# Kernel optimization log

Hardware: AMD Instinct MI355X
Metric: run time of the kernel (lower is better)

## Reference

```python
import jax, jax.numpy as jnp
import numpy as np

B, N, E = 128, 256, 2048
BINS = 16

def _gcn(x, src, dst, W, b):
    # GCNConv with self-loops and symmetric deg^-1/2 normalization (PyG default).
    h = x @ W  # [N, Fout]
    deg = jnp.zeros(x.shape[0], x.dtype).at[dst].add(1.0) + 1.0  # +1 self-loop
    dinv = jax.lax.rsqrt(deg)
    coef = dinv[src] * dinv[dst]  # [E]
    agg = jnp.zeros_like(h).at[dst].add(h[src] * coef[:, None])
    return agg + h / deg[:, None] + b  # self-loop norm = 1/deg

def _gnn(x, ei, W1, b1, W2, b2, W3, b3):
    # x: [B,N,Fin], ei: [B,2,E]. Dropout skipped (eval mode).
    def single(x, ei):
        s, d = ei[0], ei[1]
        h = jax.nn.relu(_gcn(x, s, d, W1, b1))
        h = jax.nn.relu(_gcn(h, s, d, W2, b2))
        return _gcn(h, s, d, W3, b3)
    return jax.vmap(single)(x, ei)

def _att_pool(x, Watt):
    # SimGNN attention pooling; all graphs have exactly N nodes.
    ctx = jnp.tanh((x @ Watt.T).sum(axis=1) / jnp.asarray(N, x.dtype))  # [B,f3]
    scores = jax.nn.sigmoid(jnp.einsum('bnf,bf->bn', x, ctx))  # [B,N]
    return jnp.einsum('bnf,bn->bf', x, scores)  # [B,f3]

def _forward(xq, xc, eq, ec, W1, b1, W2, b2, W3, b3, Watt, ntnW, ntnV, ntnb, fc1W, fc1b, fc2W, fc2b):
    q = _gnn(xq, eq, W1, b1, W2, b2, W3, b3)  # [B,N,f3]
    c = _gnn(xc, ec, W1, b1, W2, b2, W3, b3)
    e1 = _att_pool(q, Watt)
    e2 = _att_pool(c, Watt)
    # NTN: bilinear + linear on concat + bias
    scores = jax.nn.relu(
        jnp.einsum('bi,tij,bj->bt', e1, ntnW, e2)
        + jnp.concatenate([e1, e2], axis=-1) @ ntnV.T
        + ntnb
    )  # [B, tensor_neurons]
    # histogram of all pairwise node-embedding dot products (torch.histc semantics)
    s = jnp.einsum('bnf,bmf->bnm', q, c).ravel()
    lo, hi = s.min(), s.max()
    idx = jnp.clip(jnp.floor((s - lo) / (hi - lo) * BINS).astype(jnp.int32), 0, BINS - 1)
    counts = jnp.zeros(BINS, s.dtype).at[idx].add(1.0)
    h = jax.lax.stop_gradient(counts / counts.sum())
    scores = jnp.concatenate([scores, jnp.broadcast_to(h, (scores.shape[0], BINS))], axis=1)
    scores = jax.nn.relu(scores @ fc1W.T + fc1b)
    p = jax.nn.sigmoid(scores @ fc2W.T + fc2b)  # [B,1]
    return p.squeeze()


def setup_inputs() -> dict:
    key = jax.random.key(0)
    ks = jax.random.split(key, 20)
    Fin, f1, f2, f3, T, BN = 128, 128, 64, 32, 16, 16
    def xav(k, shape):
        fan_in, fan_out = shape[-1], shape[0]
        lim = np.sqrt(6.0 / (fan_in + fan_out))
        return jax.random.uniform(k, shape, jnp.float32, -lim, lim)
    return {
        'xq': jax.random.normal(ks[0], (B, N, Fin), jnp.float32),
        'xc': jax.random.normal(ks[1], (B, N, Fin), jnp.float32),
        'eq': jax.random.randint(ks[2], (B, 2, E), 0, N, jnp.int32),
        'ec': jax.random.randint(ks[3], (B, 2, E), 0, N, jnp.int32),
        'W1': xav(ks[4], (Fin, f1)), 'b1': jnp.zeros((f1,), jnp.float32),
        'W2': xav(ks[5], (f1, f2)), 'b2': jnp.zeros((f2,), jnp.float32),
        'W3': xav(ks[6], (f2, f3)), 'b3': jnp.zeros((f3,), jnp.float32),
        'Watt': xav(ks[7], (f3, f3)),
        'ntnW': xav(ks[8], (T, f3, f3)),
        'ntnV': xav(ks[9], (T, 2 * f3)),
        'ntnb': xav(ks[10], (T, 1)).squeeze(-1),
        'fc1W': xav(ks[11], (BN, T + BINS)), 'fc1b': jnp.zeros((BN,), jnp.float32),
        'fc2W': xav(ks[12], (1, BN)), 'fc2b': jnp.zeros((1,), jnp.float32),
    }


def reference(xq, xc, eq, ec, W1, b1, W2, b2, W3, b3, Watt, ntnW, ntnV, ntnb, fc1W, fc1b, fc2W, fc2b):
    return _forward(xq, xc, eq, ec, W1, b1, W2, b2, W3, b3, Watt, ntnW, ntnV, ntnb, fc1W, fc1b, fc2W, fc2b)
```

## Files before the change

### kernel.cpp

```cpp
#include <hip/hip_runtime.h>
#include <math.h>

#define BB 128
#define NN 256
#define EE 2048
#define BINS 16

typedef unsigned short u16;

__global__ void csr_kernel(const int* __restrict__ eq, const int* __restrict__ ec,
                           int* __restrict__ off, u16* __restrict__ srcs,
                           float* __restrict__ dvsg) {
    int g = blockIdx.x;
    int b = g < BB ? g : g - BB;
    const int* ei = g < BB ? eq : ec;
    int t = threadIdx.x;
    __shared__ int cnt[NN];
    __shared__ int sa[NN], sb[NN];
    __shared__ int cursor[NN];
    cnt[t] = 0;
    __syncthreads();
    const int* src = ei + b * 2 * EE;
    const int* dst = src + EE;
    for (int e = t; e < EE; e += 256) atomicAdd(&cnt[dst[e]], 1);
    __syncthreads();
    dvsg[g * NN + t] = rsqrtf((float)cnt[t] + 1.0f);
    sa[t] = cnt[t];
    __syncthreads();
    int* pin = sa; int* pout = sb;
    for (int d = 1; d < NN; d <<= 1) {
        int v = pin[t];
        if (t >= d) v += pin[t - d];
        pout[t] = v;
        __syncthreads();
        int* tmp = pin; pin = pout; pout = tmp;
    }
    int excl = pin[t] - cnt[t];
    off[g * 257 + t] = excl;
    if (t == 255) off[g * 257 + 256] = EE;
    cursor[t] = excl;
    __syncthreads();
    for (int e = t; e < EE; e += 256) {
        int d = dst[e], s = src[e];
        int pos = atomicAdd(&cursor[d], 1);
        srcs[g * EE + pos] = (u16)s;
    }
}

template<int FIN, int FOUT, bool RELU, int NSPLIT>
__global__ __launch_bounds__(512) void gcn_fused4(
        const float* __restrict__ X0, const float* __restrict__ X1,
        const float* __restrict__ W, const float* __restrict__ bias,
        const int* __restrict__ off, const u16* __restrict__ srcs,
        const float* __restrict__ dvsg, float* __restrict__ OUT) {
    constexpr int CHUNKS = FOUT / 32;
    int blk = blockIdx.x;
    int g = blk % (2 * BB);
    int rest = blk / (2 * BB);
    int cb = (rest % CHUNKS) * 32;
    int half = rest / CHUNKS;
    int t = threadIdx.x;

    __shared__ float uni[NN * 33];
    __shared__ int   eoff[NN + 1];
    __shared__ u16   esrc[EE];
    __shared__ float dvs_s[NN];
    float* xsT = uni;
    float* wt  = uni + 16 * 260;
    float* hT  = uni;

    const float* xg = (g < BB) ? (X0 + (size_t)g * NN * FIN)
                               : (X1 + (size_t)(g - BB) * NN * FIN);
    const int* o = off + g * 257;
    const u16* sr = srcs + (size_t)g * EE;

    for (int i = t; i < EE; i += 512) esrc[i] = sr[i];
    for (int i = t; i <= NN; i += 512) eoff[i] = o[i];
    if (t < NN) dvs_s[t] = dvsg[g * NN + t];

    int l = t & 63;
    int wv = t >> 6;

    float acc[4][4];
#pragma unroll
    for (int i = 0; i < 4; i++)
#pragma unroll
        for (int j = 0; j < 4; j++) acc[i][j] = 0.f;

    int sn = t >> 1, qk = (t & 1) * 8;
    const float* xr = xg + sn * FIN + qk;
    float4 v0 = *(const float4*)xr;
    float4 v1 = *(const float4*)(xr + 4);
    float wreg = W[(t >> 5) * FOUT + cb + (t & 31)];

    for (int k0 = 0; k0 < FIN; k0 += 16) {
        xsT[(qk + 0) * 260 + sn] = v0.x;
        xsT[(qk + 1) * 260 + sn] = v0.y;
        xsT[(qk + 2) * 260 + sn] = v0.z;
        xsT[(qk + 3) * 260 + sn] = v0.w;
        xsT[(qk + 4) * 260 + sn] = v1.x;
        xsT[(qk + 5) * 260 + sn] = v1.y;
        xsT[(qk + 6) * 260 + sn] = v1.z;
        xsT[(qk + 7) * 260 + sn] = v1.w;
        wt[t] = wreg;
        __syncthreads();
        if (k0 + 16 < FIN) {
            xr += 16;
            v0 = *(const float4*)xr;
            v1 = *(const float4*)(xr + 4);
            wreg = W[(k0 + 16 + (t >> 5)) * FOUT + cb + (t & 31)];
        }
#pragma unroll
        for (int k = 0; k < 16; k++) {
            float4 xv = *(const float4*)&xsT[k * 260 + 4 * l];
            float4 wvv = *(const float4*)&wt[k * 32 + 4 * wv];
            acc[0][0] += xv.x * wvv.x; acc[0][1] += xv.x * wvv.y;
            acc[0][2] += xv.x * wvv.z; acc[0][3] += xv.x * wvv.w;
            acc[1][0] += xv.y * wvv.x; acc[1][1] += xv.y * wvv.y;
            acc[1][2] += xv.y * wvv.z; acc[1][3] += xv.y * wvv.w;
            acc[2][0] += xv.z * wvv.x; acc[2][1] += xv.z * wvv.y;
            acc[2][2] += xv.z * wvv.z; acc[2][3] += xv.z * wvv.w;
            acc[3][0] += xv.w * wvv.x; acc[3][1] += xv.w * wvv.y;
            acc[3][2] += xv.w * wvv.z; acc[3][3] += xv.w * wvv.w;
        }
        __syncthreads();
    }
#pragma unroll
    for (int i = 0; i < 4; i++)
#pragma unroll
        for (int j = 0; j < 4; j++)
            hT[(4 * l + i) * 33 + 4 * wv + j] = acc[i][j];
    __syncthreads();

    int c = t & 31, ng = t >> 5;
    float bb_ = bias[cb + c];
    float* outp = OUT + (size_t)g * NN * FOUT;
    constexpr int NSEG = NN / NSPLIT;
    int nlo = half * NSEG, nhi = nlo + NSEG;
    for (int n = nlo + ng; n < nhi; n += 16) {
        int j0 = eoff[n], j1 = eoff[n + 1];
        float dn = dvs_s[n];
        float a = 0.f;
        int j = j0;
        for (; j + 1 < j1; j += 2) {
            int s0 = esrc[j], s1 = esrc[j + 1];
            a += hT[s0 * 33 + c] * (dvs_s[s0] * dn);
            a += hT[s1 * 33 + c] * (dvs_s[s1] * dn);
        }
        if (j < j1) {
            int s0 = esrc[j];
            a += hT[s0 * 33 + c] * (dvs_s[s0] * dn);
        }
        float d0i = 1.0f / ((float)(j1 - j0) + 1.0f);
        float val = a + hT[n * 33 + c] * d0i + bb_;
        if (RELU) val = fmaxf(val, 0.f);
        outp[n * FOUT + cb + c] = val;
    }
}

__global__ void attpool_kernel(const float* __restrict__ X, const float* __restrict__ Watt,
                               float* __restrict__ e) {
    int g = blockIdx.x;
    int t = threadIdx.x;
    __shared__ float xs[NN * 33];
    __shared__ float red[256];
    __shared__ float mean_s[32], ctx_s[32], sc[NN];
    const float* x = X + (size_t)g * NN * 32;
    for (int i = t; i < NN * 32; i += 256) { int n = i >> 5, c = i & 31; xs[n * 33 + c] = x[i]; }
    __syncthreads();
    {
        int c = t & 31, p = t >> 5;
        float s = 0.f;
        for (int n = p * 32; n < (p + 1) * 32; n++) s += xs[n * 33 + c];
        red[t] = s;
    }
    __syncthreads();
    if (t < 32) {
        float m = 0.f;
        for (int p = 0; p < 8; p++) m += red[p * 32 + t];
        mean_s[t] = m / (float)NN;
    }
    __syncthreads();
    if (t < 32) {
        float a = 0.f;
        for (int f = 0; f < 32; f++) a += mean_s[f] * Watt[t * 32 + f];
        ctx_s[t] = tanhf(a);
    }
    __syncthreads();
    {
        float a = 0.f;
        for (int f = 0; f < 32; f++) a += xs[t * 33 + f] * ctx_s[f];
        sc[t] = 1.f / (1.f + expf(-a));
    }
    __syncthreads();
    {
        int c = t & 31, p = t >> 5;
        float s = 0.f;
        for (int n = p * 32; n < (p + 1) * 32; n++) s += xs[n * 33 + c] * sc[n];
        red[t] = s;
    }
    __syncthreads();
    if (t < 32) {
        float s = 0.f;
        for (int p = 0; p < 8; p++) s += red[p * 32 + t];
        e[g * 32 + t] = s;
    }
}

#define PD_STAGE_AND_DOT \
    int blk = blockIdx.x; \
    int b = blk >> 2; \
    int tq = (blk >> 1) & 1, tc = blk & 1; \
    __shared__ float qsT[32 * 132]; \
    __shared__ float csT[32 * 132]; \
    int t = threadIdx.x; \
    { \
        int n = t >> 1, f0 = (t & 1) * 16; \
        const float* qp = Q + ((size_t)b * NN + tq * 128 + n) * 32 + f0; \
        const float* cp = C + ((size_t)b * NN + tc * 128 + n) * 32 + f0; \
        float qa16[16], ca16[16]; \
        *(float4*)&qa16[0]  = *(const float4*)(qp); \
        *(float4*)&qa16[4]  = *(const float4*)(qp + 4); \
        *(float4*)&qa16[8]  = *(const float4*)(qp + 8); \
        *(float4*)&qa16[12] = *(const float4*)(qp + 12); \
        *(float4*)&ca16[0]  = *(const float4*)(cp); \
        *(float4*)&ca16[4]  = *(const float4*)(cp + 4); \
        *(float4*)&ca16[8]  = *(const float4*)(cp + 8); \
        *(float4*)&ca16[12] = *(const float4*)(cp + 12); \
        _Pragma("unroll") \
        for (int m = 0; m < 16; m++) { \
            qsT[(f0 + m) * 132 + n] = qa16[m]; \
            csT[(f0 + m) * 132 + n] = ca16[m]; \
        } \
    } \
    __syncthreads(); \
    int rg = (t >> 4) * 4, cg = (t & 15) * 4; \
    float acc[8][8]; \
    _Pragma("unroll") \
    for (int i = 0; i < 8; i++) \
        _Pragma("unroll") \
        for (int j = 0; j < 8; j++) acc[i][j] = 0.f; \
    _Pragma("unroll 2") \
    for (int f = 0; f < 32; f++) { \
        float4 qa = *(const float4*)&qsT[f * 132 + rg]; \
        float4 qb = *(const float4*)&qsT[f * 132 + 64 + rg]; \
        float4 ca = *(const float4*)&csT[f * 132 + cg]; \
        float4 cb = *(const float4*)&csT[f * 132 + 64 + cg]; \
        float qv[8] = {qa.x, qa.y, qa.z, qa.w, qb.x, qb.y, qb.z, qb.w}; \
        float cv[8] = {ca.x, ca.y, ca.z, ca.w, cb.x, cb.y, cb.z, cb.w}; \
        _Pragma("unroll") \
        for (int i = 0; i < 8; i++) \
            _Pragma("unroll") \
            for (int j = 0; j < 8; j++) acc[i][j] += qv[i] * cv[j]; \
    }

__global__ __launch_bounds__(256, 4) void pairdot_minmax(
        const float* __restrict__ Q, const float* __restrict__ C,
        float* __restrict__ bmin, float* __restrict__ bmax) {
    PD_STAGE_AND_DOT
    float lmin = acc[0][0], lmax = acc[0][0];
#pragma unroll
    for (int i = 0; i < 8; i++)
#pragma unroll
        for (int j = 0; j < 8; j++) {
            lmin = fminf(lmin, acc[i][j]);
            lmax = fmaxf(lmax, acc[i][j]);
        }
    __shared__ float rmin[256], rmax[256];
    rmin[t] = lmin; rmax[t] = lmax;
    __syncthreads();
    for (int s = 128; s > 0; s >>= 1) {
        if (t < s) { rmin[t] = fminf(rmin[t], rmin[t + s]); rmax[t] = fmaxf(rmax[t], rmax[t + s]); }
        __syncthreads();
    }
    if (t == 0) { bmin[blk] = rmin[0]; bmax[blk] = rmax[0]; }
}

__global__ void minmax_kernel(const float* __restrict__ bmin, const float* __restrict__ bmax,
                              float* __restrict__ lohi, float* __restrict__ counts) {
    __shared__ float rmin[256], rmax[256];
    int t = threadIdx.x;
    float lmin = 1e30f, lmax = -1e30f;
    for (int i = t; i < 512; i += 256) { lmin = fminf(lmin, bmin[i]); lmax = fmaxf(lmax, bmax[i]); }
    rmin[t] = lmin; rmax[t] = lmax;
    __syncthreads();
    for (int s = 128; s > 0; s >>= 1) {
        if (t < s) { rmin[t] = fminf(rmin[t], rmin[t + s]); rmax[t] = fmaxf(rmax[t], rmax[t + s]); }
        __syncthreads();
    }
    if (t == 0) { lohi[0] = rmin[0]; lohi[1] = rmax[0]; }
    if (t < BINS) counts[t] = 0.f;
}

__global__ __launch_bounds__(256, 4) void pairdot_hist(
        const float* __restrict__ Q, const float* __restrict__ C,
        const float* __restrict__ lohi, float* __restrict__ counts) {
    PD_STAGE_AND_DOT
    float lo = lohi[0], hi = lohi[1];
    float scale = (float)BINS / (hi - lo);
    int lane = t & 63;
    int cnt = 0;
#pragma unroll
    for (int i = 0; i < 8; i++)
#pragma unroll
        for (int j = 0; j < 8; j++) {
            int idx = (int)floorf((acc[i][j] - lo) * scale);
            idx = min(max(idx, 0), BINS - 1);
            unsigned long long b0 = __ballot((idx & 1) != 0);
            unsigned long long b1 = __ballot((idx & 2) != 0);
            unsigned long long b2 = __ballot((idx & 4) != 0);
            unsigned long long b3 = __ballot((idx & 8) != 0);
            unsigned long long msk = ((lane & 1) ? b0 : ~b0);
            msk &= ((lane & 2) ? b1 : ~b1);
            msk &= ((lane & 4) ? b2 : ~b2);
            msk &= ((lane & 8) ? b3 : ~b3);
            cnt += __popcll(msk);
        }
    __shared__ float wbins[4][BINS];
    int wave = t >> 6;
    if (lane < BINS) wbins[wave][lane] = (float)cnt;
    __syncthreads();
    if (t < BINS) {
        atomicAdd(&counts[t], wbins[0][t] + wbins[1][t] + wbins[2][t] + wbins[3][t]);
    }
}

__global__ void final_kernel(const float* __restrict__ e1, const float* __restrict__ e2,
                             const float* __restrict__ ntnW, const float* __restrict__ ntnV,
                             const float* __restrict__ ntnb, const float* __restrict__ counts,
                             const float* __restrict__ fc1W, const float* __restrict__ fc1b,
                             const float* __restrict__ fc2W, const float* __restrict__ fc2b,
                             float* __restrict__ out) {
    int b = blockIdx.x;
    int t = threadIdx.x;
    __shared__ float a1[32], a2[32], red[256], z[32], u[16];
    if (t < 32) a1[t] = e1[b * 32 + t];
    else if (t < 64) a2[t - 32] = e2[b * 32 + t - 32];
    __syncthreads();
    int tt = t >> 4, g = t & 15;
    float p = 0.f;
#pragma unroll
    for (int ii = 0; ii < 2; ii++) {
        int i = g + 16 * ii;
        float d = 0.f;
        const float* wr = ntnW + (tt * 32 + i) * 32;
        for (int j = 0; j < 32; j++) d += wr[j] * a2[j];
        p += a1[i] * d;
    }
    red[t] = p;
    __syncthreads();
    if (t < 16) {
        float s = 0.f;
        for (int g2 = 0; g2 < 16; g2++) s += red[t * 16 + g2];
        float lin = ntnb[t];
        for (int i = 0; i < 32; i++) lin += ntnV[t * 64 + i] * a1[i];
        for (int i = 0; i < 32; i++) lin += ntnV[t * 64 + 32 + i] * a2[i];
        z[t] = fmaxf(s + lin, 0.f);
    } else if (t < 32) {
        float tot = 0.f;
        for (int i = 0; i < BINS; i++) tot += counts[i];
        z[t] = counts[t - 16] / tot;
    }
    __syncthreads();
    if (t < 16) {
        float a = fc1b[t];
        for (int i = 0; i < 32; i++) a += fc1W[t * 32 + i] * z[i];
        u[t] = fmaxf(a, 0.f);
    }
    __syncthreads();
    if (t == 0) {
        float a = fc2b[0];
        for (int i = 0; i < 16; i++) a += fc2W[i] * u[i];
        out[b] = 1.f / (1.f + expf(-a));
    }
}

extern "C" void kernel_launch(void* const* d_in, const int* in_sizes, int n_in,
                              void* d_out, int out_size, void* d_ws, size_t ws_size,
                              hipStream_t stream) {
    const float* xq   = (const float*)d_in[0];
    const float* xc   = (const float*)d_in[1];
    const int*   eq   = (const int*)d_in[2];
    const int*   ec   = (const int*)d_in[3];
    const float* W1   = (const float*)d_in[4];
    const float* b1   = (const float*)d_in[5];
    const float* W2   = (const float*)d_in[6];
    const float* b2   = (const float*)d_in[7];
    const float* W3   = (const float*)d_in[8];
    const float* b3   = (const float*)d_in[9];
    const float* Watt = (const float*)d_in[10];
    const float* ntnW = (const float*)d_in[11];
    const float* ntnV = (const float*)d_in[12];
    const float* ntnb = (const float*)d_in[13];
    const float* fc1W = (const float*)d_in[14];
    const float* fc1b = (const float*)d_in[15];
    const float* fc2W = (const float*)d_in[16];
    const float* fc2b = (const float*)d_in[17];
    float* out = (float*)d_out;
    float* ws  = (float*)d_ws;

    float* O3   = ws;
    float* e12  = O3 + 2097152;
    float* bmin = e12 + 8192;
    float* bmax = bmin + 2048;
    float* lohi = bmax + 2048;
    float* cntw = lohi + 2;
    int*   off  = (int*)(ws + 2109504);
    u16*   srcs = (u16*)(off + 65792);
    float* dvsg = ws + 2437440;
    float* O1   = ws + 3223872;
    float* O2   = O1 + 8388608;

    float* O3Q = O3;
    float* O3C = O3 + (size_t)BB * NN * 32;
    float* e1w = e12;
    float* e2w = e12 + BB * 32;

    csr_kernel<<<2 * BB, 256, 0, stream>>>(eq, ec, off, srcs, dvsg);

    gcn_fused4<128, 128, true, 1><<<4 * 2 * BB, 512, 0, stream>>>(
        xq, xc, W1, b1, off, srcs, dvsg, O1);
    gcn_fused4<128, 64, true, 1><<<2 * 2 * BB, 512, 0, stream>>>(
        O1, O1 + (size_t)BB * NN * 128, W2, b2, off, srcs, dvsg, O2);
    gcn_fused4<64, 32, false, 2><<<2 * 2 * BB, 512, 0, stream>>>(
        O2, O2 + (size_t)BB * NN * 64, W3, b3, off, srcs, dvsg, O3);

    attpool_kernel<<<2 * BB, 256, 0, stream>>>(O3, Watt, e12);

    pairdot_minmax<<<BB * 4, 256, 0, stream>>>(O3Q, O3C, bmin, bmax);
    minmax_kernel<<<1, 256, 0, stream>>>(bmin, bmax, lohi, cntw);
    pairdot_hist<<<BB * 4, 256, 0, stream>>>(O3Q, O3C, lohi, cntw);

    final_kernel<<<BB, 256, 0, stream>>>(e1w, e2w, ntnW, ntnV, ntnb, cntw,
                                         fc1W, fc1b, fc2W, fc2b, out);
}
```

Measured before the change: 299.5 us.

## Widen GCN output chunk per block to cut redundant X GEMM reloads

Generalizes the fused GCN kernel to a configurable output-column chunk (64 instead of 32), so each block computes more output columns per load of X and layers 1 and 2 re-read the input fewer times. Layer 2 and 3 change how the aggregation work is split across blocks (more node splits), which recomputes the full GEMM in more blocks for layer 3 and layer 2. Larger chunks double register accumulators and shared memory, which may reduce occupancy.

Result: slower. 334.6 us (+11.7%).

```diff
diff --git a/kernel.cpp b/kernel.cpp
--- a/kernel.cpp
+++ b/kernel.cpp
@@ -47,21 +47,24 @@
     }
 }
 
-template<int FIN, int FOUT, bool RELU, int NSPLIT>
-__global__ __launch_bounds__(512) void gcn_fused4(
+template<int FIN, int FOUT, int CHUNK, bool RELU, int NSPLIT>
+__global__ __launch_bounds__(512) void gcn_fused5(
         const float* __restrict__ X0, const float* __restrict__ X1,
         const float* __restrict__ W, const float* __restrict__ bias,
         const int* __restrict__ off, const u16* __restrict__ srcs,
         const float* __restrict__ dvsg, float* __restrict__ OUT) {
-    constexpr int CHUNKS = FOUT / 32;
+    constexpr int CHUNKS = FOUT / CHUNK;
+    constexpr int CPW = CHUNK / 8;
+    constexpr int NPANEL = CHUNK / 32;
+    constexpr int PSTR = NN * 33;
     int blk = blockIdx.x;
     int g = blk % (2 * BB);
     int rest = blk / (2 * BB);
-    int cb = (rest % CHUNKS) * 32;
+    int cb = (rest % CHUNKS) * CHUNK;
     int half = rest / CHUNKS;
     int t = threadIdx.x;
 
-    __shared__ float uni[NN * 33];
+    __shared__ float uni[PSTR * NPANEL];
     __shared__ int   eoff[NN + 1];
     __shared__ u16   esrc[EE];
     __shared__ float dvs_s[NN];
@@ -81,17 +84,27 @@
     int l = t & 63;
     int wv = t >> 6;
 
-    float acc[4][4];
+    float acc[4][CPW];
 #pragma unroll
     for (int i = 0; i < 4; i++)
 #pragma unroll
-        for (int j = 0; j < 4; j++) acc[i][j] = 0.f;
+        for (int j = 0; j < CPW; j++) acc[i][j] = 0.f;
 
     int sn = t >> 1, qk = (t & 1) * 8;
     const float* xr = xg + sn * FIN + qk;
     float4 v0 = *(const float4*)xr;
     float4 v1 = *(const float4*)(xr + 4);
-    float wreg = W[(t >> 5) * FOUT + cb + (t & 31)];
+
+    constexpr int EPT = CHUNK / 32;
+    int wrow = t >> 5;
+    int wcol = (t & 31) * EPT;
+    float wreg[EPT];
+    if (EPT == 2) {
+        float2 w2 = *(const float2*)&W[(size_t)wrow * FOUT + cb + wcol];
+        wreg[0] = w2.x; wreg[1] = w2.y;
+    } else {
+        wreg[0] = W[(size_t)wrow * FOUT + cb + wcol];
+    }
 
     for (int k0 = 0; k0 < FIN; k0 += 16) {
         xsT[(qk + 0) * 260 + sn] = v0.x;
@@ -102,57 +115,72 @@
         xsT[(qk + 5) * 260 + sn] = v1.y;
         xsT[(qk + 6) * 260 + sn] = v1.z;
         xsT[(qk + 7) * 260 + sn] = v1.w;
-        wt[t] = wreg;
+        if (EPT == 2) *(float2*)&wt[wrow * CHUNK + wcol] = make_float2(wreg[0], wreg[1]);
+        else          wt[wrow * CHUNK + wcol] = wreg[0];
         __syncthreads();
         if (k0 + 16 < FIN) {
             xr += 16;
             v0 = *(const float4*)xr;
             v1 = *(const float4*)(xr + 4);
-            wreg = W[(k0 + 16 + (t >> 5)) * FOUT + cb + (t & 31)];
+            if (EPT == 2) {
+                float2 w2 = *(const float2*)&W[(size_t)(k0 + 16 + wrow) * FOUT + cb + wcol];
+                wreg[0] = w2.x; wreg[1] = w2.y;
+            } else {
+                wreg[0] = W[(size_t)(k0 + 16 + wrow) * FOUT + cb + wcol];
+            }
         }
 #pragma unroll
         for (int k = 0; k < 16; k++) {
             float4 xv = *(const float4*)&xsT[k * 260 + 4 * l];
-            float4 wvv = *(const float4*)&wt[k * 32 + 4 * wv];
-            acc[0][0] += xv.x * wvv.x; acc[0][1] += xv.x * wvv.y;
-            acc[0][2] += xv.x * wvv.z; acc[0][3] += xv.x * wvv.w;
-            acc[1][0] += xv.y * wvv.x; acc[1][1] += xv.y * wvv.y;
-            acc[1][2] += xv.y * wvv.z; acc[1][3] += xv.y * wvv.w;
-            acc[2][0] += xv.z * wvv.x; acc[2][1] += xv.z * wvv.y;
-            acc[2][2] += xv.z * wvv.z; acc[2][3] += xv.z * wvv.w;
-            acc[3][0] += xv.w * wvv.x; acc[3][1] += xv.w * wvv.y;
-            acc[3][2] += xv.w * wvv.z; acc[3][3] += xv.w * wvv.w;
+            float wc[CPW];
+#pragma unroll
+            for (int j4 = 0; j4 < CPW; j4 += 4) {
+                float4 w4 = *(const float4*)&wt[k * CHUNK + CPW * wv + j4];
+                wc[j4] = w4.x; wc[j4 + 1] = w4.y; wc[j4 + 2] = w4.z; wc[j4 + 3] = w4.w;
+            }
+            float xq4[4] = {xv.x, xv.y, xv.z, xv.w};
+#pragma unroll
+            for (int i = 0; i < 4; i++)
+#pragma unroll
+                for (int j = 0; j < CPW; j++) acc[i][j] += xq4[i] * wc[j];
         }
         __syncthreads();
     }
-#pragma unroll
-    for (int i = 0; i < 4; i++)
-#pragma unroll
-        for (int j = 0; j < 4; j++)
-            hT[(4 * l + i) * 33 + 4 * wv + j] = acc[i][j];
-    __syncthreads();
-
-    int c = t & 31, ng = t >> 5;
+    {
+        int colg = CPW * wv;
+        int p = colg >> 5, cw = colg & 31;
+#pragma unroll
+        for (int i = 0; i < 4; i++)
+#pragma unroll
+            for (int j4 = 0; j4 < CPW; j4 += 4)
+                *(float4*)&hT[p * PSTR + (4 * l + i) * 33 + cw + j4] =
+                    make_float4(acc[i][j4], acc[i][j4 + 1], acc[i][j4 + 2], acc[i][j4 + 3]);
+    }
+    __syncthreads();
+
+    constexpr int NG = 512 / CHUNK;
+    int c = t & (CHUNK - 1), ng = t / CHUNK;
+    int cp = c >> 5, cc = c & 31;
     float bb_ = bias[cb + c];
     float* outp = OUT + (size_t)g * NN * FOUT;
     constexpr int NSEG = NN / NSPLIT;
     int nlo = half * NSEG, nhi = nlo + NSEG;
-    for (int n = nlo + ng; n < nhi; n += 16) {
+    for (int n = nlo + ng; n < nhi; n += NG) {
         int j0 = eoff[n], j1 = eoff[n + 1];
         float dn = dvs_s[n];
         float a = 0.f;
         int j = j0;
         for (; j + 1 < j1; j += 2) {
             int s0 = esrc[j], s1 = esrc[j + 1];
-            a += hT[s0 * 33 + c] * (dvs_s[s0] * dn);
-            a += hT[s1 * 33 + c] * (dvs_s[s1] * dn);
+            a += hT[cp * PSTR + s0 * 33 + cc] * (dvs_s[s0] * dn);
+            a += hT[cp * PSTR + s1 * 33 + cc] * (dvs_s[s1] * dn);
         }
         if (j < j1) {
             int s0 = esrc[j];
-            a += hT[s0 * 33 + c] * (dvs_s[s0] * dn);
+            a += hT[cp * PSTR + s0 * 33 + cc] * (dvs_s[s0] * dn);
         }
         float d0i = 1.0f / ((float)(j1 - j0) + 1.0f);
-        float val = a + hT[n * 33 + c] * d0i + bb_;
+        float val = a + hT[cp * PSTR + n * 33 + cc] * d0i + bb_;
         if (RELU) val = fmaxf(val, 0.f);
         outp[n * FOUT + cb + c] = val;
     }
@@ -418,11 +446,11 @@
 
     csr_kernel<<<2 * BB, 256, 0, stream>>>(eq, ec, off, srcs, dvsg);
 
-    gcn_fused4<128, 128, true, 1><<<4 * 2 * BB, 512, 0, stream>>>(
+    gcn_fused5<128, 128, 64, true, 1><<<2 * 2 * BB, 512, 0, stream>>>(
         xq, xc, W1, b1, off, srcs, dvsg, O1);
-    gcn_fused4<128, 64, true, 1><<<2 * 2 * BB, 512, 0, stream>>>(
+    gcn_fused5<128, 64, 64, true, 2><<<2 * 2 * BB, 512, 0, stream>>>(
         O1, O1 + (size_t)BB * NN * 128, W2, b2, off, srcs, dvsg, O2);
-    gcn_fused4<64, 32, false, 2><<<2 * 2 * BB, 512, 0, stream>>>(
+    gcn_fused5<64, 32, 32, false, 4><<<4 * 2 * BB, 512, 0, stream>>>(
         O2, O2 + (size_t)BB * NN * 64, W3, b3, off, srcs, dvsg, O3);
 
     attpool_kernel<<<2 * BB, 256, 0, stream>>>(O3, Watt, e12);
```

## Double-buffer GCN GEMM staging and precompute per-edge normalization weights

Applied to the files above, without the earlier changes.

The GCN transform loop now keeps two shared-memory stages and prefetches global tiles two steps ahead in registers. This lets staging of the next tile overlap compute on the current one and removes a barrier per step. Separately, the CSR build kernel precomputes each edge's dinv[src]*dinv[dst] weight into a per-graph array, so the aggregation does one shared read instead of two lookups plus a multiply. The cost is more shared memory, more live registers and a larger edge-weight buffer in the workspace.

Measured after the change: 299.6 us. No clear change (+0.0%).

```diff
diff --git a/kernel.cpp b/kernel.cpp
--- a/kernel.cpp
+++ b/kernel.cpp
@@ -10,7 +10,7 @@
 
 __global__ void csr_kernel(const int* __restrict__ eq, const int* __restrict__ ec,
                            int* __restrict__ off, u16* __restrict__ srcs,
-                           float* __restrict__ dvsg) {
+                           float* __restrict__ wts) {
     int g = blockIdx.x;
     int b = g < BB ? g : g - BB;
     const int* ei = g < BB ? eq : ec;
@@ -18,13 +18,14 @@
     __shared__ int cnt[NN];
     __shared__ int sa[NN], sb[NN];
     __shared__ int cursor[NN];
+    __shared__ float dvs[NN];
     cnt[t] = 0;
     __syncthreads();
     const int* src = ei + b * 2 * EE;
     const int* dst = src + EE;
     for (int e = t; e < EE; e += 256) atomicAdd(&cnt[dst[e]], 1);
     __syncthreads();
-    dvsg[g * NN + t] = rsqrtf((float)cnt[t] + 1.0f);
+    dvs[t] = rsqrtf((float)cnt[t] + 1.0f);
     sa[t] = cnt[t];
     __syncthreads();
     int* pin = sa; int* pout = sb;
@@ -44,16 +45,19 @@
         int d = dst[e], s = src[e];
         int pos = atomicAdd(&cursor[d], 1);
         srcs[g * EE + pos] = (u16)s;
+        wts[g * EE + pos] = dvs[s] * dvs[d];
     }
 }
 
 template<int FIN, int FOUT, bool RELU, int NSPLIT>
-__global__ __launch_bounds__(512) void gcn_fused4(
+__global__ __launch_bounds__(512) void gcn_fused6(
         const float* __restrict__ X0, const float* __restrict__ X1,
         const float* __restrict__ W, const float* __restrict__ bias,
         const int* __restrict__ off, const u16* __restrict__ srcs,
-        const float* __restrict__ dvsg, float* __restrict__ OUT) {
+        const float* __restrict__ wts, float* __restrict__ OUT) {
     constexpr int CHUNKS = FOUT / 32;
+    constexpr int NW = FIN / 16;
+    constexpr int BUF = 16 * 260 + 16 * 32;
     int blk = blockIdx.x;
     int g = blk % (2 * BB);
     int rest = blk / (2 * BB);
@@ -61,22 +65,20 @@
     int half = rest / CHUNKS;
     int t = threadIdx.x;
 
-    __shared__ float uni[NN * 33];
+    __shared__ float uni[2 * BUF];
     __shared__ int   eoff[NN + 1];
     __shared__ u16   esrc[EE];
-    __shared__ float dvs_s[NN];
-    float* xsT = uni;
-    float* wt  = uni + 16 * 260;
-    float* hT  = uni;
+    __shared__ float ewt[EE];
+    float* hT = uni;
 
     const float* xg = (g < BB) ? (X0 + (size_t)g * NN * FIN)
                                : (X1 + (size_t)(g - BB) * NN * FIN);
     const int* o = off + g * 257;
     const u16* sr = srcs + (size_t)g * EE;
-
-    for (int i = t; i < EE; i += 512) esrc[i] = sr[i];
+    const float* wg = wts + (size_t)g * EE;
+
+    for (int i = t; i < EE; i += 512) { esrc[i] = sr[i]; ewt[i] = wg[i]; }
     for (int i = t; i <= NN; i += 512) eoff[i] = o[i];
-    if (t < NN) dvs_s[t] = dvsg[g * NN + t];
 
     int l = t & 63;
     int wv = t >> 6;
@@ -89,31 +91,58 @@
 
     int sn = t >> 1, qk = (t & 1) * 8;
     const float* xr = xg + sn * FIN + qk;
-    float4 v0 = *(const float4*)xr;
-    float4 v1 = *(const float4*)(xr + 4);
-    float wreg = W[(t >> 5) * FOUT + cb + (t & 31)];
-
-    for (int k0 = 0; k0 < FIN; k0 += 16) {
-        xsT[(qk + 0) * 260 + sn] = v0.x;
-        xsT[(qk + 1) * 260 + sn] = v0.y;
-        xsT[(qk + 2) * 260 + sn] = v0.z;
-        xsT[(qk + 3) * 260 + sn] = v0.w;
-        xsT[(qk + 4) * 260 + sn] = v1.x;
-        xsT[(qk + 5) * 260 + sn] = v1.y;
-        xsT[(qk + 6) * 260 + sn] = v1.z;
-        xsT[(qk + 7) * 260 + sn] = v1.w;
-        wt[t] = wreg;
-        __syncthreads();
-        if (k0 + 16 < FIN) {
-            xr += 16;
-            v0 = *(const float4*)xr;
-            v1 = *(const float4*)(xr + 4);
-            wreg = W[(k0 + 16 + (t >> 5)) * FOUT + cb + (t & 31)];
+    int wrow = t >> 5, wcol = t & 31;
+
+    auto stage = [&](float* buf, const float4& s0, const float4& s1, float sw) {
+        buf[(qk + 0) * 260 + sn] = s0.x;
+        buf[(qk + 1) * 260 + sn] = s0.y;
+        buf[(qk + 2) * 260 + sn] = s0.z;
+        buf[(qk + 3) * 260 + sn] = s0.w;
+        buf[(qk + 4) * 260 + sn] = s1.x;
+        buf[(qk + 5) * 260 + sn] = s1.y;
+        buf[(qk + 6) * 260 + sn] = s1.z;
+        buf[(qk + 7) * 260 + sn] = s1.w;
+        buf[16 * 260 + t] = sw;
+    };
+
+    float4 rA0 = *(const float4*)(xr);
+    float4 rA1 = *(const float4*)(xr + 4);
+    float  wA  = W[(size_t)wrow * FOUT + cb + wcol];
+    float4 rB0 = *(const float4*)(xr + 16);
+    float4 rB1 = *(const float4*)(xr + 20);
+    float  wB  = W[(size_t)(16 + wrow) * FOUT + cb + wcol];
+    stage(uni, rA0, rA1, wA);
+    if (NW > 2) {
+        rA0 = *(const float4*)(xr + 32);
+        rA1 = *(const float4*)(xr + 36);
+        wA  = W[(size_t)(32 + wrow) * FOUT + cb + wcol];
+    }
+    __syncthreads();
+
+#pragma unroll
+    for (int it = 0; it < NW; ++it) {
+        float* cur = uni + (it & 1) * BUF;
+        if (it + 1 < NW) {
+            float* nb = uni + ((it + 1) & 1) * BUF;
+            if (((it + 1) & 1) == 0) stage(nb, rA0, rA1, wA);
+            else                     stage(nb, rB0, rB1, wB);
+            if (it + 3 < NW) {
+                int ko = (it + 3) * 16;
+                if (((it + 3) & 1) == 0) {
+                    rA0 = *(const float4*)(xr + ko);
+                    rA1 = *(const float4*)(xr + ko + 4);
+                    wA  = W[(size_t)(ko + wrow) * FOUT + cb + wcol];
+                } else {
+                    rB0 = *(const float4*)(xr + ko);
+                    rB1 = *(const float4*)(xr + ko + 4);
+                    wB  = W[(size_t)(ko + wrow) * FOUT + cb + wcol];
+                }
+            }
         }
 #pragma unroll
         for (int k = 0; k < 16; k++) {
-            float4 xv = *(const float4*)&xsT[k * 260 + 4 * l];
-            float4 wvv = *(const float4*)&wt[k * 32 + 4 * wv];
+            float4 xv  = *(const float4*)&cur[k * 260 + 4 * l];
+            float4 wvv = *(const float4*)&cur[16 * 260 + k * 32 + 4 * wv];
             acc[0][0] += xv.x * wvv.x; acc[0][1] += xv.x * wvv.y;
             acc[0][2] += xv.x * wvv.z; acc[0][3] += xv.x * wvv.w;
             acc[1][0] += xv.y * wvv.x; acc[1][1] += xv.y * wvv.y;
@@ -139,17 +168,15 @@
     int nlo = half * NSEG, nhi = nlo + NSEG;
     for (int n = nlo + ng; n < nhi; n += 16) {
         int j0 = eoff[n], j1 = eoff[n + 1];
-        float dn = dvs_s[n];
         float a = 0.f;
         int j = j0;
         for (; j + 1 < j1; j += 2) {
             int s0 = esrc[j], s1 = esrc[j + 1];
-            a += hT[s0 * 33 + c] * (dvs_s[s0] * dn);
-            a += hT[s1 * 33 + c] * (dvs_s[s1] * dn);
+            a += hT[s0 * 33 + c] * ewt[j];
+            a += hT[s1 * 33 + c] * ewt[j + 1];
         }
         if (j < j1) {
-            int s0 = esrc[j];
-            a += hT[s0 * 33 + c] * (dvs_s[s0] * dn);
+            a += hT[esrc[j] * 33 + c] * ewt[j];
         }
         float d0i = 1.0f / ((float)(j1 - j0) + 1.0f);
         float val = a + hT[n * 33 + c] * d0i + bb_;
@@ -407,7 +434,7 @@
     float* cntw = lohi + 2;
     int*   off  = (int*)(ws + 2109504);
     u16*   srcs = (u16*)(off + 65792);
-    float* dvsg = ws + 2437440;
+    float* wts  = ws + 2437440;
     float* O1   = ws + 3223872;
     float* O2   = O1 + 8388608;
 
@@ -416,14 +443,14 @@
     float* e1w = e12;
     float* e2w = e12 + BB * 32;
 
-    csr_kernel<<<2 * BB, 256, 0, stream>>>(eq, ec, off, srcs, dvsg);
-
-    gcn_fused4<128, 128, true, 1><<<4 * 2 * BB, 512, 0, stream>>>(
-        xq, xc, W1, b1, off, srcs, dvsg, O1);
-    gcn_fused4<128, 64, true, 1><<<2 * 2 * BB, 512, 0, stream>>>(
-        O1, O1 + (size_t)BB * NN * 128, W2, b2, off, srcs, dvsg, O2);
-    gcn_fused4<64, 32, false, 2><<<2 * 2 * BB, 512, 0, stream>>>(
-        O2, O2 + (size_t)BB * NN * 64, W3, b3, off, srcs, dvsg, O3);
+    csr_kernel<<<2 * BB, 256, 0, stream>>>(eq, ec, off, srcs, wts);
+
+    gcn_fused6<128, 128, true, 1><<<4 * 2 * BB, 512, 0, stream>>>(
+        xq, xc, W1, b1, off, srcs, wts, O1);
+    gcn_fused6<128, 64, true, 1><<<2 * 2 * BB, 512, 0, stream>>>(
+        O1, O1 + (size_t)BB * NN * 128, W2, b2, off, srcs, wts, O2);
+    gcn_fused6<64, 32, false, 2><<<2 * 2 * BB, 512, 0, stream>>>(
+        O2, O2 + (size_t)BB * NN * 64, W3, b3, off, srcs, wts, O3);
 
     attpool_kernel<<<2 * BB, 256, 0, stream>>>(O3, Watt, e12);
 
```

## Fuse all three GCN layers into one per-graph kernel with precomputed edge weights

Applied to the files above, without the earlier changes.

The three separate GCN layer launches are replaced by a single 1024-thread block per graph. That block computes X@W1, aggregation, X@W2, aggregation, X@W3 and the final aggregation, keeping the intermediate activations in registers and shared memory instead of writing O1 and O2 to global memory. The CSR kernel now precomputes per-edge normalisation weights dinv[s]*dinv[d], which removes the per-edge multiply and the lookup during aggregation. The cost is lower grid parallelism: 256 blocks instead of up to 2048, with heavy shared memory and register use per block, which may limit occupancy.

After: 757.0 us. 2.53x slower.

```diff
diff --git a/kernel.cpp b/kernel.cpp
--- a/kernel.cpp
+++ b/kernel.cpp
@@ -10,7 +10,7 @@
 
 __global__ void csr_kernel(const int* __restrict__ eq, const int* __restrict__ ec,
                            int* __restrict__ off, u16* __restrict__ srcs,
-                           float* __restrict__ dvsg) {
+                           float* __restrict__ wts) {
     int g = blockIdx.x;
     int b = g < BB ? g : g - BB;
     const int* ei = g < BB ? eq : ec;
@@ -18,13 +18,14 @@
     __shared__ int cnt[NN];
     __shared__ int sa[NN], sb[NN];
     __shared__ int cursor[NN];
+    __shared__ float dvs[NN];
     cnt[t] = 0;
     __syncthreads();
     const int* src = ei + b * 2 * EE;
     const int* dst = src + EE;
     for (int e = t; e < EE; e += 256) atomicAdd(&cnt[dst[e]], 1);
     __syncthreads();
-    dvsg[g * NN + t] = rsqrtf((float)cnt[t] + 1.0f);
+    dvs[t] = rsqrtf((float)cnt[t] + 1.0f);
     sa[t] = cnt[t];
     __syncthreads();
     int* pin = sa; int* pout = sb;
@@ -44,117 +45,219 @@
         int d = dst[e], s = src[e];
         int pos = atomicAdd(&cursor[d], 1);
         srcs[g * EE + pos] = (u16)s;
-    }
-}
-
-template<int FIN, int FOUT, bool RELU, int NSPLIT>
-__global__ __launch_bounds__(512) void gcn_fused4(
-        const float* __restrict__ X0, const float* __restrict__ X1,
-        const float* __restrict__ W, const float* __restrict__ bias,
+        wts[g * EE + pos] = dvs[s] * dvs[d];
+    }
+}
+
+__global__ __launch_bounds__(1024) void gcn_all(
+        const float* __restrict__ XQ, const float* __restrict__ XC,
+        const float* __restrict__ W1, const float* __restrict__ b1,
+        const float* __restrict__ W2, const float* __restrict__ b2,
+        const float* __restrict__ W3, const float* __restrict__ b3,
         const int* __restrict__ off, const u16* __restrict__ srcs,
-        const float* __restrict__ dvsg, float* __restrict__ OUT) {
-    constexpr int CHUNKS = FOUT / 32;
-    int blk = blockIdx.x;
-    int g = blk % (2 * BB);
-    int rest = blk / (2 * BB);
-    int cb = (rest % CHUNKS) * 32;
-    int half = rest / CHUNKS;
+        const float* __restrict__ wts, float* __restrict__ O3) {
+    int g = blockIdx.x;
     int t = threadIdx.x;
 
-    __shared__ float uni[NN * 33];
+    __shared__ float Hb[NN * 67];
+    __shared__ float xsT[16 * 260];
+    __shared__ float wts_s[16 * 64];
     __shared__ int   eoff[NN + 1];
     __shared__ u16   esrc[EE];
-    __shared__ float dvs_s[NN];
-    float* xsT = uni;
-    float* wt  = uni + 16 * 260;
-    float* hT  = uni;
-
-    const float* xg = (g < BB) ? (X0 + (size_t)g * NN * FIN)
-                               : (X1 + (size_t)(g - BB) * NN * FIN);
-    const int* o = off + g * 257;
-    const u16* sr = srcs + (size_t)g * EE;
-
-    for (int i = t; i < EE; i += 512) esrc[i] = sr[i];
-    for (int i = t; i <= NN; i += 512) eoff[i] = o[i];
-    if (t < NN) dvs_s[t] = dvsg[g * NN + t];
+    __shared__ float ewt[EE];
+
+    const float* xg = (g < BB) ? (XQ + (size_t)g * NN * 128)
+                               : (XC + (size_t)(g - BB) * NN * 128);
+    {
+        const int* o = off + g * 257;
+        const u16* sre = srcs + (size_t)g * EE;
+        const float* wge = wts + (size_t)g * EE;
+        for (int i = t; i < EE; i += 1024) { esrc[i] = sre[i]; ewt[i] = wge[i]; }
+        if (t <= NN) eoff[t] = o[t];
+    }
 
     int l = t & 63;
     int wv = t >> 6;
-
-    float acc[4][4];
-#pragma unroll
-    for (int i = 0; i < 4; i++)
-#pragma unroll
-        for (int j = 0; j < 4; j++) acc[i][j] = 0.f;
-
-    int sn = t >> 1, qk = (t & 1) * 8;
-    const float* xr = xg + sn * FIN + qk;
-    float4 v0 = *(const float4*)xr;
-    float4 v1 = *(const float4*)(xr + 4);
-    float wreg = W[(t >> 5) * FOUT + cb + (t & 31)];
-
-    for (int k0 = 0; k0 < FIN; k0 += 16) {
-        xsT[(qk + 0) * 260 + sn] = v0.x;
-        xsT[(qk + 1) * 260 + sn] = v0.y;
-        xsT[(qk + 2) * 260 + sn] = v0.z;
-        xsT[(qk + 3) * 260 + sn] = v0.w;
-        xsT[(qk + 4) * 260 + sn] = v1.x;
-        xsT[(qk + 5) * 260 + sn] = v1.y;
-        xsT[(qk + 6) * 260 + sn] = v1.z;
-        xsT[(qk + 7) * 260 + sn] = v1.w;
-        wt[t] = wreg;
+    int sr_ = t >> 2;
+    int sq  = (t & 3) * 4;
+    int wr16 = t >> 6, wc64 = t & 63;
+    int gc = t & 63, gng = t >> 6;
+    const float* xrow = xg + sr_ * 128 + sq;
+
+    float a1[2][16];
+    float a2[16];
+
+#pragma unroll
+    for (int hf = 0; hf < 2; ++hf) {
+        const int cb = hf * 64;
+        float acc[4][4];
+#pragma unroll
+        for (int i = 0; i < 4; i++)
+#pragma unroll
+            for (int j = 0; j < 4; j++) acc[i][j] = 0.f;
+        float4 xv4 = *(const float4*)(xrow);
+        float wreg = W1[(size_t)wr16 * 128 + cb + wc64];
+        for (int k0 = 0; k0 < 128; k0 += 16) {
+            xsT[(sq + 0) * 260 + sr_] = xv4.x;
+            xsT[(sq + 1) * 260 + sr_] = xv4.y;
+            xsT[(sq + 2) * 260 + sr_] = xv4.z;
+            xsT[(sq + 3) * 260 + sr_] = xv4.w;
+            wts_s[t] = wreg;
+            __syncthreads();
+            if (k0 + 16 < 128) {
+                xv4 = *(const float4*)(xrow + k0 + 16);
+                wreg = W1[(size_t)(k0 + 16 + wr16) * 128 + cb + wc64];
+            }
+#pragma unroll
+            for (int k = 0; k < 16; k++) {
+                float4 xv = *(const float4*)&xsT[k * 260 + 4 * l];
+                float4 wvv = *(const float4*)&wts_s[k * 64 + 4 * wv];
+                acc[0][0] += xv.x * wvv.x; acc[0][1] += xv.x * wvv.y;
+                acc[0][2] += xv.x * wvv.z; acc[0][3] += xv.x * wvv.w;
+                acc[1][0] += xv.y * wvv.x; acc[1][1] += xv.y * wvv.y;
+                acc[1][2] += xv.y * wvv.z; acc[1][3] += xv.y * wvv.w;
+                acc[2][0] += xv.z * wvv.x; acc[2][1] += xv.z * wvv.y;
+                acc[2][2] += xv.z * wvv.z; acc[2][3] += xv.z * wvv.w;
+                acc[3][0] += xv.w * wvv.x; acc[3][1] += xv.w * wvv.y;
+                acc[3][2] += xv.w * wvv.z; acc[3][3] += xv.w * wvv.w;
+            }
+            __syncthreads();
+        }
+#pragma unroll
+        for (int i = 0; i < 4; i++)
+#pragma unroll
+            for (int j = 0; j < 4; j++)
+                Hb[(4 * l + i) * 67 + 4 * wv + j] = acc[i][j];
         __syncthreads();
-        if (k0 + 16 < FIN) {
-            xr += 16;
-            v0 = *(const float4*)xr;
-            v1 = *(const float4*)(xr + 4);
-            wreg = W[(k0 + 16 + (t >> 5)) * FOUT + cb + (t & 31)];
-        }
-#pragma unroll
-        for (int k = 0; k < 16; k++) {
-            float4 xv = *(const float4*)&xsT[k * 260 + 4 * l];
-            float4 wvv = *(const float4*)&wt[k * 32 + 4 * wv];
-            acc[0][0] += xv.x * wvv.x; acc[0][1] += xv.x * wvv.y;
-            acc[0][2] += xv.x * wvv.z; acc[0][3] += xv.x * wvv.w;
-            acc[1][0] += xv.y * wvv.x; acc[1][1] += xv.y * wvv.y;
-            acc[1][2] += xv.y * wvv.z; acc[1][3] += xv.y * wvv.w;
-            acc[2][0] += xv.z * wvv.x; acc[2][1] += xv.z * wvv.y;
-            acc[2][2] += xv.z * wvv.z; acc[2][3] += xv.z * wvv.w;
-            acc[3][0] += xv.w * wvv.x; acc[3][1] += xv.w * wvv.y;
-            acc[3][2] += xv.w * wvv.z; acc[3][3] += xv.w * wvv.w;
-        }
+        float bb_ = b1[cb + gc];
+#pragma unroll
+        for (int i = 0; i < 16; i++) {
+            int n = gng + 16 * i;
+            int j0 = eoff[n], j1 = eoff[n + 1];
+            float a = 0.f;
+            int j = j0;
+            for (; j + 1 < j1; j += 2) {
+                int s0 = esrc[j], s1 = esrc[j + 1];
+                a += Hb[s0 * 67 + gc] * ewt[j];
+                a += Hb[s1 * 67 + gc] * ewt[j + 1];
+            }
+            if (j < j1) a += Hb[esrc[j] * 67 + gc] * ewt[j];
+            float d0i = 1.0f / ((float)(j1 - j0) + 1.0f);
+            float v = a + Hb[n * 67 + gc] * d0i + bb_;
+            a1[hf][i] = fmaxf(v, 0.f);
+        }
+    }
+
+    {
+        float acc[4][4];
+#pragma unroll
+        for (int i = 0; i < 4; i++)
+#pragma unroll
+            for (int j = 0; j < 4; j++) acc[i][j] = 0.f;
+        float wreg = W2[(size_t)wr16 * 64 + wc64];
+#pragma unroll
+        for (int jt = 0; jt < 8; ++jt) {
+            if ((gc >> 4) == (jt & 3)) {
+                int cr = gc - (jt & 3) * 16;
+#pragma unroll
+                for (int i = 0; i < 16; i++)
+                    xsT[cr * 260 + gng + 16 * i] = (jt < 4) ? a1[0][i] : a1[1][i];
+            }
+            wts_s[t] = wreg;
+            __syncthreads();
+            if (jt + 1 < 8) wreg = W2[(size_t)((jt + 1) * 16 + wr16) * 64 + wc64];
+#pragma unroll
+            for (int k = 0; k < 16; k++) {
+                float4 xv = *(const float4*)&xsT[k * 260 + 4 * l];
+                float4 wvv = *(const float4*)&wts_s[k * 64 + 4 * wv];
+                acc[0][0] += xv.x * wvv.x; acc[0][1] += xv.x * wvv.y;
+                acc[0][2] += xv.x * wvv.z; acc[0][3] += xv.x * wvv.w;
+                acc[1][0] += xv.y * wvv.x; acc[1][1] += xv.y * wvv.y;
+                acc[1][2] += xv.y * wvv.z; acc[1][3] += xv.y * wvv.w;
+                acc[2][0] += xv.z * wvv.x; acc[2][1] += xv.z * wvv.y;
+                acc[2][2] += xv.z * wvv.z; acc[2][3] += xv.z * wvv.w;
+                acc[3][0] += xv.w * wvv.x; acc[3][1] += xv.w * wvv.y;
+                acc[3][2] += xv.w * wvv.z; acc[3][3] += xv.w * wvv.w;
+            }
+            __syncthreads();
+        }
+#pragma unroll
+        for (int i = 0; i < 4; i++)
+#pragma unroll
+            for (int j = 0; j < 4; j++)
+                Hb[(4 * l + i) * 67 + 4 * wv + j] = acc[i][j];
         __syncthreads();
-    }
-#pragma unroll
-    for (int i = 0; i < 4; i++)
-#pragma unroll
-        for (int j = 0; j < 4; j++)
-            hT[(4 * l + i) * 33 + 4 * wv + j] = acc[i][j];
-    __syncthreads();
-
-    int c = t & 31, ng = t >> 5;
-    float bb_ = bias[cb + c];
-    float* outp = OUT + (size_t)g * NN * FOUT;
-    constexpr int NSEG = NN / NSPLIT;
-    int nlo = half * NSEG, nhi = nlo + NSEG;
-    for (int n = nlo + ng; n < nhi; n += 16) {
-        int j0 = eoff[n], j1 = eoff[n + 1];
-        float dn = dvs_s[n];
-        float a = 0.f;
-        int j = j0;
-        for (; j + 1 < j1; j += 2) {
-            int s0 = esrc[j], s1 = esrc[j + 1];
-            a += hT[s0 * 33 + c] * (dvs_s[s0] * dn);
-            a += hT[s1 * 33 + c] * (dvs_s[s1] * dn);
-        }
-        if (j < j1) {
-            int s0 = esrc[j];
-            a += hT[s0 * 33 + c] * (dvs_s[s0] * dn);
-        }
-        float d0i = 1.0f / ((float)(j1 - j0) + 1.0f);
-        float val = a + hT[n * 33 + c] * d0i + bb_;
-        if (RELU) val = fmaxf(val, 0.f);
-        outp[n * FOUT + cb + c] = val;
+        float bb_ = b2[gc];
+#pragma unroll
+        for (int i = 0; i < 16; i++) {
+            int n = gng + 16 * i;
+            int j0 = eoff[n], j1 = eoff[n + 1];
+            float a = 0.f;
+            int j = j0;
+            for (; j + 1 < j1; j += 2) {
+                int s0 = esrc[j], s1 = esrc[j + 1];
+                a += Hb[s0 * 67 + gc] * ewt[j];
+                a += Hb[s1 * 67 + gc] * ewt[j + 1];
+            }
+            if (j < j1) a += Hb[esrc[j] * 67 + gc] * ewt[j];
+            float d0i = 1.0f / ((float)(j1 - j0) + 1.0f);
+            float v = a + Hb[n * 67 + gc] * d0i + bb_;
+            a2[i] = fmaxf(v, 0.f);
+        }
+    }
+
+    {
+        float acc3[4][2];
+#pragma unroll
+        for (int i = 0; i < 4; i++) { acc3[i][0] = 0.f; acc3[i][1] = 0.f; }
+        float wreg3 = (t < 512) ? W3[(size_t)(t >> 5) * 32 + (t & 31)] : 0.f;
+#pragma unroll
+        for (int jt = 0; jt < 4; ++jt) {
+            if ((gc >> 4) == jt) {
+                int cr = gc - jt * 16;
+#pragma unroll
+                for (int i = 0; i < 16; i++)
+                    xsT[cr * 260 + gng + 16 * i] = a2[i];
+            }
+            if (t < 512) wts_s[t] = wreg3;
+            __syncthreads();
+            if (jt + 1 < 4 && t < 512)
+                wreg3 = W3[(size_t)((jt + 1) * 16 + (t >> 5)) * 32 + (t & 31)];
+#pragma unroll
+            for (int k = 0; k < 16; k++) {
+                float4 xv = *(const float4*)&xsT[k * 260 + 4 * l];
+                float2 wvv = *(const float2*)&wts_s[k * 32 + 2 * wv];
+                acc3[0][0] += xv.x * wvv.x; acc3[0][1] += xv.x * wvv.y;
+                acc3[1][0] += xv.y * wvv.x; acc3[1][1] += xv.y * wvv.y;
+                acc3[2][0] += xv.z * wvv.x; acc3[2][1] += xv.z * wvv.y;
+                acc3[3][0] += xv.w * wvv.x; acc3[3][1] += xv.w * wvv.y;
+            }
+            __syncthreads();
+        }
+#pragma unroll
+        for (int i = 0; i < 4; i++) {
+            Hb[(4 * l + i) * 67 + 2 * wv + 0] = acc3[i][0];
+            Hb[(4 * l + i) * 67 + 2 * wv + 1] = acc3[i][1];
+        }
+        __syncthreads();
+        int c3 = t & 31, ng3 = t >> 5;
+        float bb_ = b3[c3];
+        float* outp = O3 + (size_t)g * NN * 32;
+#pragma unroll
+        for (int i = 0; i < 8; i++) {
+            int n = ng3 + 32 * i;
+            int j0 = eoff[n], j1 = eoff[n + 1];
+            float a = 0.f;
+            int j = j0;
+            for (; j + 1 < j1; j += 2) {
+                int s0 = esrc[j], s1 = esrc[j + 1];
+                a += Hb[s0 * 67 + c3] * ewt[j];
+                a += Hb[s1 * 67 + c3] * ewt[j + 1];
+            }
+            if (j < j1) a += Hb[esrc[j] * 67 + c3] * ewt[j];
+            float d0i = 1.0f / ((float)(j1 - j0) + 1.0f);
+            outp[n * 32 + c3] = a + Hb[n * 67 + c3] * d0i + bb_;
+        }
     }
 }
 
@@ -407,23 +510,17 @@
     float* cntw = lohi + 2;
     int*   off  = (int*)(ws + 2109504);
     u16*   srcs = (u16*)(off + 65792);
-    float* dvsg = ws + 2437440;
-    float* O1   = ws + 3223872;
-    float* O2   = O1 + 8388608;
+    float* wts  = ws + 2437440;
 
     float* O3Q = O3;
     float* O3C = O3 + (size_t)BB * NN * 32;
     float* e1w = e12;
     float* e2w = e12 + BB * 32;
 
-    csr_kernel<<<2 * BB, 256, 0, stream>>>(eq, ec, off, srcs, dvsg);
-
-    gcn_fused4<128, 128, true, 1><<<4 * 2 * BB, 512, 0, stream>>>(
-        xq, xc, W1, b1, off, srcs, dvsg, O1);
-    gcn_fused4<128, 64, true, 1><<<2 * 2 * BB, 512, 0, stream>>>(
-        O1, O1 + (size_t)BB * NN * 128, W2, b2, off, srcs, dvsg, O2);
-    gcn_fused4<64, 32, false, 2><<<2 * 2 * BB, 512, 0, stream>>>(
-        O2, O2 + (size_t)BB * NN * 64, W3, b3, off, srcs, dvsg, O3);
+    csr_kernel<<<2 * BB, 256, 0, stream>>>(eq, ec, off, srcs, wts);
+
+    gcn_all<<<2 * BB, 1024, 0, stream>>>(xq, xc, W1, b1, W2, b2, W3, b3,
+                                         off, srcs, wts, O3);
 
     attpool_kernel<<<2 * BB, 256, 0, stream>>>(O3, Watt, e12);
 
```
